# Optimization experiments

Hardware: AMD Instinct MI355X
Metric: run time of the kernel (lower is better)

Reference implementation:

```python
import jax, jax.numpy as jnp
import numpy as np

B, D, H, W = 4, 64, 64, 64
MODES = 8
WIDTH = 32
N_LAYERS = 4


def setup_inputs() -> dict:
    key = jax.random.key(0)
    ks = jax.random.split(key, 20)
    C = WIDTH
    m = MODES
    spec_scale = 1.0 / (C * C)
    inp = {
        "velocity_model": jax.random.normal(ks[0], (B, 1, D, H, W), jnp.float32),
        "partial_travel_time": jax.random.normal(ks[1], (B, 1, D, H, W), jnp.float32),
        "lift_w": jax.random.normal(ks[2], (2, C), jnp.float32) * 0.5,
        "lift_b": jax.random.normal(ks[3], (C,), jnp.float32) * 0.1,
        "spec_wr": jax.random.normal(ks[4], (N_LAYERS, 4, C, C, m, m, m), jnp.float32) * spec_scale,
        "spec_wi": jax.random.normal(ks[5], (N_LAYERS, 4, C, C, m, m, m), jnp.float32) * spec_scale,
        "skip_w": jax.random.normal(ks[6], (N_LAYERS, C, C), jnp.float32) * (1.0 / np.sqrt(C)),
        "skip_b": jax.random.normal(ks[7], (N_LAYERS, C), jnp.float32) * 0.1,
        "proj_w": jax.random.normal(ks[8], (C, C), jnp.float32) * (1.0 / np.sqrt(C)),
        "proj_b": jax.random.normal(ks[9], (C,), jnp.float32) * 0.1,
        "fc1_w": jax.random.normal(ks[10], (C, 128), jnp.float32) * (1.0 / np.sqrt(C)),
        "fc1_b": jax.random.normal(ks[11], (128,), jnp.float32) * 0.1,
        "fc2_w": jax.random.normal(ks[12], (128, 64), jnp.float32) * (1.0 / np.sqrt(128)),
        "fc2_b": jax.random.normal(ks[13], (64,), jnp.float32) * 0.1,
        "fc3_w": jax.random.normal(ks[14], (64, 3), jnp.float32) * (1.0 / np.sqrt(64)),
        "fc3_b": jax.random.normal(ks[15], (3,), jnp.float32) * 0.1,
    }
    return inp


def _spectral_conv3d(x, wr, wi, m):
    # x: [B, Cin, D, H, W] real; wr/wi: [4, Cin, Cout, m, m, m]
    b, ci, d, h, w = x.shape
    co = wr.shape[2]
    xf = jnp.fft.rfftn(x, axes=(-3, -2, -1))  # [B, Cin, D, H, W//2+1] complex
    wc = wr + 1j * wi
    lo = slice(None, m)
    hi = slice(-m, None)
    corners = [(lo, lo), (lo, hi), (hi, lo), (hi, hi)]
    out = jnp.zeros((b, co, d, h, w // 2 + 1), dtype=xf.dtype)
    for i, (sd, sh) in enumerate(corners):
        blk = jnp.einsum('bixyz,ioxyz->boxyz', xf[:, :, sd, sh, :m], wc[i])
        out = out.at[:, :, sd, sh, :m].set(blk)
    return jnp.fft.irfftn(out, s=(d, h, w), axes=(-3, -2, -1))


def _channel_linear(x, w, bias):
    # x: [B, Cin, D, H, W]; w: [Cin, Cout]
    return jnp.einsum('bixyz,io->boxyz', x, w) + bias[None, :, None, None, None]


def reference(velocity_model, partial_travel_time, lift_w, lift_b, spec_wr, spec_wi,
              skip_w, skip_b, proj_w, proj_b, fc1_w, fc1_b, fc2_w, fc2_b, fc3_w, fc3_b):
    # concat along channel dim -> [B, 2, D, H, W]
    x = jnp.concatenate([velocity_model, partial_travel_time], axis=1)
    # lifting to hidden width
    x = _channel_linear(x, lift_w, lift_b)
    n_layers = spec_wr.shape[0]
    for l in range(n_layers):
        y = _spectral_conv3d(x, spec_wr[l], spec_wi[l], MODES)
        s = _channel_linear(x, skip_w[l], skip_b[l])
        x = y + s
        if l < n_layers - 1:
            x = jax.nn.gelu(x)
    # projection to out_channels = width
    x = _channel_linear(x, proj_w, proj_b)
    # global spatial mean -> [B, width]
    x = jnp.mean(x, axis=(-3, -2, -1))
    # MLP head: width -> 128 -> 64 -> 3
    x = jax.nn.relu(x @ fc1_w + fc1_b)
    x = jax.nn.relu(x @ fc2_w + fc2_b)
    return x @ fc3_w + fc3_b
```

## Files before the change

### kernel.cpp

```cpp
#include <hip/hip_runtime.h>
#include <math.h>

#define NSP 262144
static constexpr float TWO_PI_OVER_64 = 0.09817477042468103f;

__global__ __launch_bounds__(256) void k_fwd_wh2(const float* __restrict__ vel,
                                                 const float* __restrict__ ptt,
                                                 float2* __restrict__ VP2) {
  __shared__ float plane[64][65];
  __shared__ float2 A[64][8];
  __shared__ float2 tw[64];
  int t = threadIdx.x;
  if (t < 64) { float s, c; sincosf(TWO_PI_OVER_64 * t, &s, &c); tw[t] = make_float2(c, s); }
  int b = blockIdx.x >> 7, ch = (blockIdx.x >> 6) & 1, d = blockIdx.x & 63;
  const float4* src = (const float4*)((ch ? ptt : vel) + (size_t)b * NSP + d * 4096);
  for (int p = 0; p < 4; ++p) {
    int i = t + 256 * p;
    float4 v = src[i];
    int h = i >> 4, sg = (i & 15) * 4;
    plane[h][sg] = v.x; plane[h][sg + 1] = v.y; plane[h][sg + 2] = v.z; plane[h][sg + 3] = v.w;
  }
  __syncthreads();
  for (int p = 0; p < 2; ++p) {
    int o = t + 256 * p;
    int h = o >> 3, kw = o & 7;
    float re = 0.f, im = 0.f;
    for (int w = 0; w < 64; ++w) {
      float2 cs = tw[(kw * w) & 63];
      float v = plane[h][w];
      re += v * cs.x; im -= v * cs.y;
    }
    A[h][kw] = make_float2(re, im);
  }
  __syncthreads();
  if (t < 128) {
    int kh = t >> 3, kw = t & 7;
    int f = (kh < 8) ? kh : kh + 48;
    float re = 0.f, im = 0.f;
    for (int h = 0; h < 64; ++h) {
      float2 cs = tw[(h * f) & 63];
      float2 a = A[h][kw];
      re += a.x * cs.x + a.y * cs.y;
      im += a.y * cs.x - a.x * cs.y;
    }
    VP2[(size_t)blockIdx.x * 128 + t] = make_float2(re, im);
  }
}

__global__ __launch_bounds__(256) void k_fwd_d_lift(const float2* __restrict__ VP2,
                                                    const float* __restrict__ lw,
                                                    const float* __restrict__ lb,
                                                    float2* __restrict__ X3) {
  __shared__ float2 tile[2][64][8];
  __shared__ float2 F[2][16][8];
  __shared__ float2 tw[64];
  int t = threadIdx.x;
  if (t < 64) { float s, c; sincosf(TWO_PI_OVER_64 * t, &s, &c); tw[t] = make_float2(c, s); }
  int b = blockIdx.x >> 4, kh = blockIdx.x & 15;
  for (int p = 0; p < 4; ++p) {
    int i = t + 256 * p;
    int ch = i >> 9, dd = (i >> 3) & 63, kw = i & 7;
    tile[ch][dd][kw] = VP2[(size_t)((b * 2 + ch) * 64 + dd) * 128 + kh * 8 + kw];
  }
  __syncthreads();
  { int ch = t >> 7, kd = (t >> 3) & 15, kw = t & 7;
    int f = (kd < 8) ? kd : kd + 48;
    float re = 0.f, im = 0.f;
    for (int dd = 0; dd < 64; ++dd) {
      float2 cs = tw[(dd * f) & 63];
      float2 v = tile[ch][dd][kw];
      re += v.x * cs.x + v.y * cs.y;
      im += v.y * cs.x - v.x * cs.y;
    }
    F[ch][kd][kw] = make_float2(re, im); }
  __syncthreads();
  for (int p = 0; p < 16; ++p) {
    int o = t + 256 * p;
    int ci = o >> 7, kd = (o >> 3) & 15, kw = o & 7;
    float2 f0 = F[0][kd][kw], f1 = F[1][kd][kw];
    float w0 = lw[ci], w1 = lw[32 + ci];
    float2 v = make_float2(w0 * f0.x + w1 * f1.x, w0 * f0.y + w1 * f1.y);
    if (kh == 0 && kd == 0 && kw == 0) v.x += lb[ci] * 262144.f;
    X3[(size_t)(b * 32 + ci) * 2048 + kd * 128 + kh * 8 + kw] = v;
  }
}

__global__ __launch_bounds__(128) void k_fwd_h(const float2* __restrict__ X1,
                                               float2* __restrict__ X2) {
  __shared__ float2 tile[64][8];
  __shared__ float2 tw[64];
  int t = threadIdx.x;
  if (t < 64) { float s, c; sincosf(TWO_PI_OVER_64 * t, &s, &c); tw[t] = make_float2(c, s); }
  const float4* s4 = (const float4*)(X1 + (size_t)blockIdx.x * 512);
  float4* t4 = (float4*)tile;
  t4[t] = s4[t];
  t4[t + 128] = s4[t + 128];
  __syncthreads();
  int kh = t >> 3, k = t & 7;
  int f = (kh < 8) ? kh : kh + 48;
  float re = 0.f, im = 0.f;
#pragma unroll 8
  for (int h = 0; h < 64; ++h) {
    float2 cs = tw[(h * f) & 63];
    float2 v = tile[h][k];
    re += v.x * cs.x + v.y * cs.y;
    im += v.y * cs.x - v.x * cs.y;
  }
  X2[(size_t)blockIdx.x * 128 + t] = make_float2(re, im);
}

__global__ __launch_bounds__(128) void k_fwd_d(const float2* __restrict__ X2,
                                               float2* __restrict__ X3) {
  __shared__ float2 tile[64][8];
  __shared__ float2 tw[64];
  int t = threadIdx.x;
  if (t < 64) { float s, c; sincosf(TWO_PI_OVER_64 * t, &s, &c); tw[t] = make_float2(c, s); }
  int kh = blockIdx.x & 15, bc = blockIdx.x >> 4;
  const float2* src = X2 + (size_t)bc * 8192 + kh * 8;
  for (int i = t; i < 512; i += 128) tile[i >> 3][i & 7] = src[(i >> 3) * 128 + (i & 7)];
  __syncthreads();
  int kd = t >> 3, k = t & 7;
  int f = (kd < 8) ? kd : kd + 48;
  float re = 0.f, im = 0.f;
#pragma unroll 8
  for (int d = 0; d < 64; ++d) {
    float2 cs = tw[(d * f) & 63];
    float2 v = tile[d][k];
    re += v.x * cs.x + v.y * cs.y;
    im += v.y * cs.x - v.x * cs.y;
  }
  X3[(size_t)bc * 2048 + kd * 128 + kh * 8 + k] = make_float2(re, im);
}

__global__ __launch_bounds__(256) void k_mix(const float2* __restrict__ X3,
                                             const float* __restrict__ wr,
                                             const float* __restrict__ wi,
                                             float2* __restrict__ Y3) {
  __shared__ float2 xs[4][32][8];
  int t = threadIdx.x;
  int kd = blockIdx.x >> 4, kh = blockIdx.x & 15;
  for (int i = t; i < 1024; i += 256) {
    int b = i >> 8, ci = (i >> 3) & 31, k = i & 7;
    xs[b][ci][k] = X3[(size_t)(b * 32 + ci) * 2048 + kd * 128 + kh * 8 + k];
  }
  __syncthreads();
  int corner = ((kd >= 8) ? 2 : 0) + ((kh >= 8) ? 1 : 0);
  int md = kd & 7, mh = kh & 7;
  int co = t >> 3, k = t & 7;
  size_t wbase = (size_t)corner * 32 * 32 * 512 + (size_t)md * 64 + (size_t)mh * 8 + k;
  float ar0 = 0, ai0 = 0, ar1 = 0, ai1 = 0, ar2 = 0, ai2 = 0, ar3 = 0, ai3 = 0;
  for (int ci = 0; ci < 32; ++ci) {
    size_t o = wbase + (size_t)(ci * 32 + co) * 512;
    float wre = wr[o], wim = wi[o];
    float2 v0 = xs[0][ci][k], v1 = xs[1][ci][k];
    float2 v2 = xs[2][ci][k], v3 = xs[3][ci][k];
    ar0 += v0.x * wre - v0.y * wim;  ai0 += v0.x * wim + v0.y * wre;
    ar1 += v1.x * wre - v1.y * wim;  ai1 += v1.x * wim + v1.y * wre;
    ar2 += v2.x * wre - v2.y * wim;  ai2 += v2.x * wim + v2.y * wre;
    ar3 += v3.x * wre - v3.y * wim;  ai3 += v3.x * wim + v3.y * wre;
  }
  size_t obase = (size_t)kd * 128 + kh * 8 + k;
  Y3[(size_t)(0 * 32 + co) * 2048 + obase] = make_float2(ar0, ai0);
  Y3[(size_t)(1 * 32 + co) * 2048 + obase] = make_float2(ar1, ai1);
  Y3[(size_t)(2 * 32 + co) * 2048 + obase] = make_float2(ar2, ai2);
  Y3[(size_t)(3 * 32 + co) * 2048 + obase] = make_float2(ar3, ai3);
}

__global__ __launch_bounds__(256) void k_inv_dh(const float2* __restrict__ Y3,
                                                float2* __restrict__ Z2) {
  __shared__ float2 yt[2048];
  __shared__ float2 zd[4][16][8];
  __shared__ float2 tw[64];
  int t = threadIdx.x;
  if (t < 64) { float s, c; sincosf(TWO_PI_OVER_64 * t, &s, &c); tw[t] = make_float2(c, s); }
  int bc = blockIdx.x >> 4, d0 = (blockIdx.x & 15) * 4;
  const float4* y4 = (const float4*)(Y3 + (size_t)bc * 2048);
  float4* yt4 = (float4*)yt;
  for (int p = 0; p < 4; ++p) yt4[t + 256 * p] = y4[t + 256 * p];
  __syncthreads();
  const float sc = 1.f / 262144.f;
  for (int p = 0; p < 2; ++p) {
    int o = t + 256 * p;
    int dd = o >> 7, kh = (o >> 3) & 15, kw = o & 7;
    int d = d0 + dd;
    float re = 0.f, im = 0.f;
#pragma unroll
    for (int kd = 0; kd < 16; ++kd) {
      int f = (kd < 8) ? kd : kd + 48;
      float2 cs = tw[(d * f) & 63];
      float2 v = yt[kd * 128 + kh * 8 + kw];
      re += v.x * cs.x - v.y * cs.y;
      im += v.x * cs.y + v.y * cs.x;
    }
    zd[dd][kh][kw] = make_float2(re * sc, im * sc);
  }
  __syncthreads();
  for (int p = 0; p < 8; ++p) {
    int o = t + 256 * p;
    int dd = o >> 9, h = (o >> 3) & 63, kw = o & 7;
    float re = 0.f, im = 0.f;
#pragma unroll
    for (int kh = 0; kh < 16; ++kh) {
      int f = (kh < 8) ? kh : kh + 48;
      float2 cs = tw[(h * f) & 63];
      float2 v = zd[dd][kh][kw];
      re += v.x * cs.x - v.y * cs.y;
      im += v.x * cs.y + v.y * cs.x;
    }
    Z2[((size_t)bc * 64 + d0 + dd) * 512 + h * 8 + kw] = make_float2(re, im);
  }
}

template <int MODE>
__global__ __launch_bounds__(256, 3) void k_tail(
    const float2* __restrict__ S, const float* __restrict__ xin,
    const float* __restrict__ pttin, const float* __restrict__ lw,
    const float* __restrict__ lb, const float* __restrict__ skw,
    const float* __restrict__ skb, float* __restrict__ xout,
    float2* __restrict__ X1out, float* __restrict__ pr) {
  __shared__ float2 tw[64];
  __shared__ float2 zt[32][2][9];
  __shared__ float sw[32][32];
  __shared__ float xt[(MODE == 0) ? 2 : 32][2][64];
  __shared__ float gt[(MODE == 2) ? 1 : 32][2][68];
  int t = threadIdx.x;
  if (t < 64) { float s, c; sincosf(TWO_PI_OVER_64 * t, &s, &c); tw[t] = make_float2(c, s); }
  int b = blockIdx.x >> 11, d = (blockIdx.x >> 5) & 63, h0 = (blockIdx.x & 31) * 2;
  {
    int co = t >> 3, hh = (t >> 2) & 1, q = t & 3;
    const float4* S4 = (const float4*)S;
    float4 v = S4[(size_t)((b * 32 + co) * 64 + d) * 256 + (h0 + hh) * 4 + q];
    zt[co][hh][2 * q] = make_float2(v.x, v.y);
    zt[co][hh][2 * q + 1] = make_float2(v.z, v.w);
  }
  if constexpr (MODE == 0) {
    if (t < 64) {
      int ch = t >> 5, hh = (t >> 4) & 1, sg = t & 15;
      const float4* src = (const float4*)(ch ? pttin : xin);
      *(float4*)&xt[ch][hh][sg * 4] =
          src[((size_t)b * NSP + d * 4096 + (h0 + hh) * 64) / 4 + sg];
    } else if (t >= 128 && t < 192) {
      int j = (t >> 5) & 1, co = t & 31;
      float a = 0.f;
      for (int ci = 0; ci < 32; ++ci) a += lw[j * 32 + ci] * skw[ci * 32 + co];
      sw[j][co] = a;
    } else if (t >= 192 && t < 224) {
      int co = t & 31;
      float a = skb[co];
      for (int ci = 0; ci < 32; ++ci) a += lb[ci] * skw[ci * 32 + co];
      sw[2][co] = a;
    }
  } else {
    { int ci = t >> 3, q = t & 7;
      *(float4*)&sw[ci][q * 4] = ((const float4*)skw)[t]; }
    for (int p = 0; p < 4; ++p) {
      int idx = t + 256 * p, row = idx >> 4, ci = row >> 1, hh = row & 1, sg = idx & 15;
      *(float4*)&xt[ci][hh][sg * 4] =
          ((const float4*)xin)[(size_t)(((b * 32 + ci) * 64 + d) * 64 + h0 + hh) * 16 + sg];
    }
  }
  __syncthreads();

  int co = t >> 3, ws = t & 7;
  float bias = (MODE == 0) ? sw[2][co] : skb[co];
  float acc[2][8];
#pragma unroll
  for (int hh = 0; hh < 2; ++hh) {
    float z0 = zt[co][hh][0].x;
#pragma unroll
    for (int j = 0; j < 8; ++j) acc[hh][j] = bias + z0;
  }
#pragma unroll
  for (int k = 1; k < 8; ++k) {
    float2 z0 = zt[co][0][k], z1 = zt[co][1][k];
#pragma unroll
    for (int j = 0; j < 8; ++j) {
      float2 cs = tw[(k * (8 * ws + j)) & 63];
      acc[0][j] += 2.f * (z0.x * cs.x - z0.y * cs.y);
      acc[1][j] += 2.f * (z1.x * cs.x - z1.y * cs.y);
    }
  }
  constexpr int NCI = (MODE == 0) ? 2 : 32;
  for (int ci = 0; ci < NCI; ++ci) {
    float s = sw[ci][co];
#pragma unroll
    for (int hh = 0; hh < 2; ++hh) {
      float4 a = *(const float4*)&xt[ci][hh][8 * ws];
      float4 c2 = *(const float4*)&xt[ci][hh][8 * ws + 4];
      acc[hh][0] += a.x * s;  acc[hh][1] += a.y * s;
      acc[hh][2] += a.z * s;  acc[hh][3] += a.w * s;
      acc[hh][4] += c2.x * s; acc[hh][5] += c2.y * s;
      acc[hh][6] += c2.z * s; acc[hh][7] += c2.w * s;
    }
  }
#pragma unroll
  for (int hh = 0; hh < 2; ++hh)
#pragma unroll
    for (int j = 0; j < 8; ++j) {
      float g = acc[hh][j];
      float u = 0.7978845608028654f * (g + 0.044715f * g * g * g);
      acc[hh][j] = __fdividef(g, 1.f + __expf(-2.f * u));
    }

  if constexpr (MODE == 2) {
    float s = 0.f;
#pragma unroll
    for (int hh = 0; hh < 2; ++hh)
#pragma unroll
      for (int j = 0; j < 8; ++j) s += acc[hh][j];
    s += __shfl_down(s, 4, 8);
    s += __shfl_down(s, 2, 8);
    s += __shfl_down(s, 1, 8);
    if (ws == 0) atomicAdd(&pr[b * 32 + co], s);
  } else {
#pragma unroll
    for (int hh = 0; hh < 2; ++hh) {
      *(float4*)&gt[co][hh][8 * ws] = make_float4(acc[hh][0], acc[hh][1], acc[hh][2], acc[hh][3]);
      *(float4*)&gt[co][hh][8 * ws + 4] = make_float4(acc[hh][4], acc[hh][5], acc[hh][6], acc[hh][7]);
    }
    __syncthreads();
    for (int p = 0; p < 4; ++p) {
      int idx = t + 256 * p, row = idx >> 4, ci = row >> 1, hh = row & 1, sg = idx & 15;
      ((float4*)xout)[(size_t)(((b * 32 + ci) * 64 + d) * 64 + h0 + hh) * 16 + sg] =
          *(float4*)&gt[ci][hh][sg * 4];
    }
    for (int p = 0; p < 2; ++p) {
      int o = t + 256 * p;
      int c2 = o >> 4, hh = (o >> 3) & 1, kw = o & 7;
      float re = 0.f, im = 0.f;
      for (int w = 0; w < 64; ++w) {
        float g = gt[c2][hh][w];
        float2 cs = tw[(kw * w) & 63];
        re += g * cs.x;
        im -= g * cs.y;
      }
      X1out[(size_t)((b * 32 + c2) * 64 + d) * 512 + (h0 + hh) * 8 + kw] = make_float2(re, im);
    }
  }
}

__global__ __launch_bounds__(128) void k_head(const float* __restrict__ pr,
                                              const float* __restrict__ swr,
                                              const float* __restrict__ skw,
                                              const float* __restrict__ skb,
                                              const float* __restrict__ pw,
                                              const float* __restrict__ pb,
                                              const float* __restrict__ f1w,
                                              const float* __restrict__ f1b,
                                              const float* __restrict__ f2w,
                                              const float* __restrict__ f2b,
                                              const float* __restrict__ f3w,
                                              const float* __restrict__ f3b,
                                              float* __restrict__ out) {
  __shared__ float m[128], h1[128], p2[128], f1[512], f2[256];
  int t = threadIdx.x;
  m[t] = pr[t] * (1.f / 262144.f);
  __syncthreads();
  { int b = t >> 5, co = t & 31;
    float acc = skb[96 + co];
    for (int ci = 0; ci < 32; ++ci) {
      float wdc = swr[((size_t)12 * 1024 + (size_t)(ci * 32 + co)) * 512];
      acc += m[b * 32 + ci] * (wdc + skw[3072 + ci * 32 + co]);
    }
    h1[t] = acc; }
  __syncthreads();
  { int b = t >> 5, o = t & 31;
    float acc = pb[o];
    for (int c = 0; c < 32; ++c) acc += h1[b * 32 + c] * pw[c * 32 + o];
    p2[t] = acc; }
  __syncthreads();
  for (int j = 0; j < 4; ++j) {
    int idx = t + 128 * j, b = idx >> 7, o = idx & 127;
    float acc = f1b[o];
    for (int c = 0; c < 32; ++c) acc += p2[b * 32 + c] * f1w[c * 128 + o];
    f1[idx] = fmaxf(acc, 0.f);
  }
  __syncthreads();
  for (int j = 0; j < 2; ++j) {
    int idx = t + 128 * j, b = idx >> 6, o = idx & 63;
    float acc = f2b[o];
    for (int c = 0; c < 128; ++c) acc += f1[b * 128 + c] * f2w[c * 64 + o];
    f2[idx] = fmaxf(acc, 0.f);
  }
  __syncthreads();
  if (t < 12) {
    int b = t / 3, o = t % 3;
    float acc = f3b[o];
    for (int c = 0; c < 64; ++c) acc += f2[b * 64 + c] * f3w[c * 3 + o];
    out[t] = acc;
  }
}

extern "C" void kernel_launch(void* const* d_in, const int* in_sizes, int n_in,
                              void* d_out, int out_size, void* d_ws, size_t ws_size,
                              hipStream_t stream) {
  const float* vel = (const float*)d_in[0];
  const float* ptt = (const float*)d_in[1];
  const float* lw  = (const float*)d_in[2];
  const float* lb  = (const float*)d_in[3];
  const float* swr = (const float*)d_in[4];
  const float* swi = (const float*)d_in[5];
  const float* skw = (const float*)d_in[6];
  const float* skb = (const float*)d_in[7];
  const float* pw  = (const float*)d_in[8];
  const float* pb  = (const float*)d_in[9];
  const float* f1w = (const float*)d_in[10];
  const float* f1b = (const float*)d_in[11];
  const float* f2w = (const float*)d_in[12];
  const float* f2b = (const float*)d_in[13];
  const float* f3w = (const float*)d_in[14];
  const float* f3b = (const float*)d_in[15];
  float* out = (float*)d_out;

  char* ws = (char*)d_ws;
  float*  x   = (float*)(ws);
  float2* S   = (float2*)(ws + 134217728ULL);
  float2* X2  = (float2*)(ws + 167772160ULL);
  float2* VP2 = X2;
  float2* X3  = (float2*)(ws + 176160768ULL);
  float2* Y3  = (float2*)(ws + 178257920ULL);
  float*  pr  = (float*)(ws + 180355072ULL);
  if (ws_size < 180355584ULL) return;

  hipMemsetAsync(pr, 0, 512, stream);

  k_fwd_wh2<<<512, 256, 0, stream>>>(vel, ptt, VP2);
  k_fwd_d_lift<<<64, 256, 0, stream>>>(VP2, lw, lb, X3);
  k_mix<<<256, 256, 0, stream>>>(X3, swr, swi, Y3);
  k_inv_dh<<<2048, 256, 0, stream>>>(Y3, S);
  k_tail<0><<<8192, 256, 0, stream>>>(S, vel, ptt, lw, lb, skw, skb, x, S, nullptr);

  k_fwd_h<<<8192, 128, 0, stream>>>(S, X2);
  k_fwd_d<<<2048, 128, 0, stream>>>(X2, X3);
  k_mix<<<256, 256, 0, stream>>>(X3, swr + 2097152, swi + 2097152, Y3);
  k_inv_dh<<<2048, 256, 0, stream>>>(Y3, S);
  k_tail<1><<<8192, 256, 0, stream>>>(S, x, nullptr, nullptr, nullptr,
                                      skw + 1024, skb + 32, x, S, nullptr);

  k_fwd_h<<<8192, 128, 0, stream>>>(S, X2);
  k_fwd_d<<<2048, 128, 0, stream>>>(X2, X3);
  k_mix<<<256, 256, 0, stream>>>(X3, swr + 2 * 2097152, swi + 2 * 2097152, Y3);
  k_inv_dh<<<2048, 256, 0, stream>>>(Y3, S);
  k_tail<2><<<8192, 256, 0, stream>>>(S, x, nullptr, nullptr, nullptr,
                                      skw + 2048, skb + 64, nullptr, nullptr, pr);

  k_head<<<1, 128, 0, stream>>>(pr, swr, skw, skb, pw, pb, f1w, f1b,
                                f2w, f2b, f3w, f3b, out);
}
```

Measured before the change: 724.2 us.

## Register-tile k_tail over 8 channels by 8 w, with shuffle-based partial DFT

Restructures the tail kernel so each thread computes an 8-channel by 8-width register tile, covering 4 h rows per block with 128 threads. Twiddles come from recurrence multiplication instead of table lookups. The forward W-DFT of the output is done in registers and reduced with warp butterfly shuffles rather than through a shared gt buffer and a 64-long loop per output. This aims to cut shared-memory traffic and per-element twiddle loads, at the cost of much higher register pressure (launch bounds 128,1) and lower occupancy.

```diff
diff --git a/kernel.cpp b/kernel.cpp
--- a/kernel.cpp
+++ b/kernel.cpp
@@ -212,129 +212,216 @@
 }
 
 template <int MODE>
-__global__ __launch_bounds__(256, 3) void k_tail(
+__global__ __launch_bounds__(128, 1) void k_tail(
     const float2* __restrict__ S, const float* __restrict__ xin,
     const float* __restrict__ pttin, const float* __restrict__ lw,
     const float* __restrict__ lb, const float* __restrict__ skw,
     const float* __restrict__ skb, float* __restrict__ xout,
-    float2* __restrict__ X1out, float* __restrict__ pr) {
-  __shared__ float2 tw[64];
-  __shared__ float2 zt[32][2][9];
-  __shared__ float sw[32][32];
-  __shared__ float xt[(MODE == 0) ? 2 : 32][2][64];
-  __shared__ float gt[(MODE == 2) ? 1 : 32][2][68];
-  int t = threadIdx.x;
-  if (t < 64) { float s, c; sincosf(TWO_PI_OVER_64 * t, &s, &c); tw[t] = make_float2(c, s); }
-  int b = blockIdx.x >> 11, d = (blockIdx.x >> 5) & 63, h0 = (blockIdx.x & 31) * 2;
+    float2* __restrict__ Sout, float* __restrict__ pr) {
+  __shared__ float2 zt[4][8][32];
+  __shared__ float xt[(MODE == 0) ? 2 : 32][4][64];
+  __shared__ float sw[(MODE == 0) ? 3 : 32][32];
+  __shared__ float2 tws[64];
+  int t = threadIdx.x;
+  if (t < 64) { float s, c; sincosf(TWO_PI_OVER_64 * t, &s, &c); tws[t] = make_float2(c, s); }
+  int b = blockIdx.x >> 10, d = (blockIdx.x >> 4) & 63, ht = blockIdx.x & 15;
+
   {
-    int co = t >> 3, hh = (t >> 2) & 1, q = t & 3;
+    int co = t >> 2, sub = t & 3;
     const float4* S4 = (const float4*)S;
-    float4 v = S4[(size_t)((b * 32 + co) * 64 + d) * 256 + (h0 + hh) * 4 + q];
-    zt[co][hh][2 * q] = make_float2(v.x, v.y);
-    zt[co][hh][2 * q + 1] = make_float2(v.z, v.w);
+    size_t base = ((size_t)(b * 32 + co) * 64 + d) * 256;
+#pragma unroll
+    for (int hl = 0; hl < 4; ++hl) {
+      float4 v = S4[base + (ht * 4 + hl) * 4 + sub];
+      zt[hl][2 * sub][co] = make_float2(v.x, v.y);
+      zt[hl][2 * sub + 1][co] = make_float2(v.z, v.w);
+    }
   }
   if constexpr (MODE == 0) {
-    if (t < 64) {
-      int ch = t >> 5, hh = (t >> 4) & 1, sg = t & 15;
+    { int ch = t >> 6, hl = (t >> 4) & 3, q = t & 15;
       const float4* src = (const float4*)(ch ? pttin : xin);
-      *(float4*)&xt[ch][hh][sg * 4] =
-          src[((size_t)b * NSP + d * 4096 + (h0 + hh) * 64) / 4 + sg];
-    } else if (t >= 128 && t < 192) {
-      int j = (t >> 5) & 1, co = t & 31;
-      float a = 0.f;
-      for (int ci = 0; ci < 32; ++ci) a += lw[j * 32 + ci] * skw[ci * 32 + co];
-      sw[j][co] = a;
-    } else if (t >= 192 && t < 224) {
-      int co = t & 31;
-      float a = skb[co];
-      for (int ci = 0; ci < 32; ++ci) a += lb[ci] * skw[ci * 32 + co];
-      sw[2][co] = a;
+      *(float4*)&xt[ch][hl][q * 4] =
+          src[(size_t)b * 65536 + d * 1024 + (ht * 4 + hl) * 16 + q]; }
+    if (t < 96) {
+      int r = t >> 5, co = t & 31;
+      if (r < 2) {
+        float a = 0.f;
+        for (int ci = 0; ci < 32; ++ci) a += lw[r * 32 + ci] * skw[ci * 32 + co];
+        sw[r][co] = a;
+      } else {
+        float a = skb[co];
+        for (int ci = 0; ci < 32; ++ci) a += lb[ci] * skw[ci * 32 + co];
+        sw[2][co] = a;
+      }
     }
   } else {
-    { int ci = t >> 3, q = t & 7;
-      *(float4*)&sw[ci][q * 4] = ((const float4*)skw)[t]; }
-    for (int p = 0; p < 4; ++p) {
-      int idx = t + 256 * p, row = idx >> 4, ci = row >> 1, hh = row & 1, sg = idx & 15;
-      *(float4*)&xt[ci][hh][sg * 4] =
-          ((const float4*)xin)[(size_t)(((b * 32 + ci) * 64 + d) * 64 + h0 + hh) * 16 + sg];
-    }
-  }
-  __syncthreads();
-
-  int co = t >> 3, ws = t & 7;
-  float bias = (MODE == 0) ? sw[2][co] : skb[co];
-  float acc[2][8];
-#pragma unroll
-  for (int hh = 0; hh < 2; ++hh) {
-    float z0 = zt[co][hh][0].x;
-#pragma unroll
-    for (int j = 0; j < 8; ++j) acc[hh][j] = bias + z0;
+    ((float4*)sw)[t] = ((const float4*)skw)[t];
+    ((float4*)sw)[t + 128] = ((const float4*)skw)[t + 128];
+    { int ci = t >> 2, q = t & 3;
+      const float4* x4 = (const float4*)xin;
+      size_t base = (((size_t)(b * 32 + ci) * 64 + d) * 64 + ht * 4) * 16;
+#pragma unroll
+      for (int hl = 0; hl < 4; ++hl)
+#pragma unroll
+        for (int j = 0; j < 4; ++j)
+          *(float4*)&xt[ci][hl][(q + 4 * j) * 4] = x4[base + hl * 16 + q + 4 * j];
+    }
+  }
+  __syncthreads();
+
+  int cg = t >> 5, hloc = (t >> 3) & 3, ws = t & 7;
+  int co0 = cg * 8, h = ht * 4 + hloc, w0 = ws * 8;
+  float2 e1[8], cur[8];
+#pragma unroll
+  for (int j = 0; j < 8; ++j) { e1[j] = tws[w0 + j]; cur[j] = e1[j]; }
+  float bias[8];
+#pragma unroll
+  for (int r = 0; r < 8; ++r)
+    bias[r] = (MODE == 0) ? sw[2][co0 + r] : skb[co0 + r];
+
+  float g[8][8];
+  {
+    const float4* zp = (const float4*)&zt[hloc][0][co0];
+    float4 a0 = zp[0], a1 = zp[1], a2 = zp[2], a3 = zp[3];
+    float z0[8] = {a0.x, a0.z, a1.x, a1.z, a2.x, a2.z, a3.x, a3.z};
+#pragma unroll
+    for (int r = 0; r < 8; ++r) {
+      float v = z0[r] + bias[r];
+#pragma unroll
+      for (int j = 0; j < 8; ++j) g[r][j] = v;
+    }
   }
 #pragma unroll
   for (int k = 1; k < 8; ++k) {
-    float2 z0 = zt[co][0][k], z1 = zt[co][1][k];
+    const float4* zp = (const float4*)&zt[hloc][k][co0];
+    float4 a0 = zp[0], a1 = zp[1], a2 = zp[2], a3 = zp[3];
+    float2 z[8] = {make_float2(a0.x, a0.y), make_float2(a0.z, a0.w),
+                   make_float2(a1.x, a1.y), make_float2(a1.z, a1.w),
+                   make_float2(a2.x, a2.y), make_float2(a2.z, a2.w),
+                   make_float2(a3.x, a3.y), make_float2(a3.z, a3.w)};
+#pragma unroll
+    for (int r = 0; r < 8; ++r)
+#pragma unroll
+      for (int j = 0; j < 8; ++j)
+        g[r][j] += 2.f * (z[r].x * cur[j].x - z[r].y * cur[j].y);
+    if (k < 7)
+#pragma unroll
+      for (int j = 0; j < 8; ++j) {
+        float cx = cur[j].x * e1[j].x - cur[j].y * e1[j].y;
+        cur[j].y = cur[j].x * e1[j].y + cur[j].y * e1[j].x;
+        cur[j].x = cx;
+      }
+  }
+  constexpr int NCI = (MODE == 0) ? 2 : 32;
+#pragma unroll
+  for (int ci = 0; ci < NCI; ++ci) {
+    float4 xa = *(const float4*)&xt[ci][hloc][w0];
+    float4 xb = *(const float4*)&xt[ci][hloc][w0 + 4];
+    float4 sa = *(const float4*)&sw[ci][co0];
+    float4 sb = *(const float4*)&sw[ci][co0 + 4];
+    float xv[8] = {xa.x, xa.y, xa.z, xa.w, xb.x, xb.y, xb.z, xb.w};
+    float sv[8] = {sa.x, sa.y, sa.z, sa.w, sb.x, sb.y, sb.z, sb.w};
+#pragma unroll
+    for (int r = 0; r < 8; ++r)
+#pragma unroll
+      for (int j = 0; j < 8; ++j) g[r][j] += xv[j] * sv[r];
+  }
+#pragma unroll
+  for (int r = 0; r < 8; ++r)
 #pragma unroll
     for (int j = 0; j < 8; ++j) {
-      float2 cs = tw[(k * (8 * ws + j)) & 63];
-      acc[0][j] += 2.f * (z0.x * cs.x - z0.y * cs.y);
-      acc[1][j] += 2.f * (z1.x * cs.x - z1.y * cs.y);
-    }
-  }
-  constexpr int NCI = (MODE == 0) ? 2 : 32;
-  for (int ci = 0; ci < NCI; ++ci) {
-    float s = sw[ci][co];
-#pragma unroll
-    for (int hh = 0; hh < 2; ++hh) {
-      float4 a = *(const float4*)&xt[ci][hh][8 * ws];
-      float4 c2 = *(const float4*)&xt[ci][hh][8 * ws + 4];
-      acc[hh][0] += a.x * s;  acc[hh][1] += a.y * s;
-      acc[hh][2] += a.z * s;  acc[hh][3] += a.w * s;
-      acc[hh][4] += c2.x * s; acc[hh][5] += c2.y * s;
-      acc[hh][6] += c2.z * s; acc[hh][7] += c2.w * s;
-    }
-  }
-#pragma unroll
-  for (int hh = 0; hh < 2; ++hh)
-#pragma unroll
-    for (int j = 0; j < 8; ++j) {
-      float g = acc[hh][j];
-      float u = 0.7978845608028654f * (g + 0.044715f * g * g * g);
-      acc[hh][j] = __fdividef(g, 1.f + __expf(-2.f * u));
+      float v = g[r][j];
+      float u = 0.7978845608028654f * (v + 0.044715f * v * v * v);
+      g[r][j] = __fdividef(v, 1.f + __expf(-2.f * u));
     }
 
   if constexpr (MODE == 2) {
-    float s = 0.f;
-#pragma unroll
-    for (int hh = 0; hh < 2; ++hh)
-#pragma unroll
-      for (int j = 0; j < 8; ++j) s += acc[hh][j];
-    s += __shfl_down(s, 4, 8);
-    s += __shfl_down(s, 2, 8);
-    s += __shfl_down(s, 1, 8);
-    if (ws == 0) atomicAdd(&pr[b * 32 + co], s);
+    float rs[8];
+#pragma unroll
+    for (int r = 0; r < 8; ++r) {
+      float s = 0.f;
+#pragma unroll
+      for (int j = 0; j < 8; ++j) s += g[r][j];
+      rs[r] = s;
+    }
+#pragma unroll
+    for (int off = 1; off < 32; off <<= 1)
+#pragma unroll
+      for (int r = 0; r < 8; ++r) rs[r] += __shfl_xor(rs[r], off, 32);
+    if ((t & 31) == 0)
+#pragma unroll
+      for (int r = 0; r < 8; ++r) atomicAdd(&pr[b * 32 + co0 + r], rs[r]);
   } else {
-#pragma unroll
-    for (int hh = 0; hh < 2; ++hh) {
-      *(float4*)&gt[co][hh][8 * ws] = make_float4(acc[hh][0], acc[hh][1], acc[hh][2], acc[hh][3]);
-      *(float4*)&gt[co][hh][8 * ws + 4] = make_float4(acc[hh][4], acc[hh][5], acc[hh][6], acc[hh][7]);
-    }
-    __syncthreads();
-    for (int p = 0; p < 4; ++p) {
-      int idx = t + 256 * p, row = idx >> 4, ci = row >> 1, hh = row & 1, sg = idx & 15;
-      ((float4*)xout)[(size_t)(((b * 32 + ci) * 64 + d) * 64 + h0 + hh) * 16 + sg] =
-          *(float4*)&gt[ci][hh][sg * 4];
-    }
-    for (int p = 0; p < 2; ++p) {
-      int o = t + 256 * p;
-      int c2 = o >> 4, hh = (o >> 3) & 1, kw = o & 7;
-      float re = 0.f, im = 0.f;
-      for (int w = 0; w < 64; ++w) {
-        float g = gt[c2][hh][w];
-        float2 cs = tw[(kw * w) & 63];
-        re += g * cs.x;
-        im -= g * cs.y;
+    float4* x4o = (float4*)xout;
+#pragma unroll
+    for (int r = 0; r < 8; ++r) {
+      size_t o = (((size_t)(b * 32 + co0 + r) * 64 + d) * 64 + h) * 16 + 2 * ws;
+      x4o[o] = make_float4(g[r][0], g[r][1], g[r][2], g[r][3]);
+      x4o[o + 1] = make_float4(g[r][4], g[r][5], g[r][6], g[r][7]);
+    }
+#pragma unroll
+    for (int half = 0; half < 2; ++half) {
+      float2 P[4][8];
+#pragma unroll
+      for (int r = 0; r < 4; ++r) {
+        float s = 0.f;
+#pragma unroll
+        for (int j = 0; j < 8; ++j) s += g[half * 4 + r][j];
+        P[r][0] = make_float2(s, 0.f);
       }
-      X1out[(size_t)((b * 32 + c2) * 64 + d) * 512 + (h0 + hh) * 8 + kw] = make_float2(re, im);
+      float2 cc[8];
+#pragma unroll
+      for (int j = 0; j < 8; ++j) cc[j] = make_float2(e1[j].x, -e1[j].y);
+#pragma unroll
+      for (int kw = 1; kw < 8; ++kw) {
+#pragma unroll
+        for (int r = 0; r < 4; ++r) {
+          float re = 0.f, im = 0.f;
+#pragma unroll
+          for (int j = 0; j < 8; ++j) {
+            re += g[half * 4 + r][j] * cc[j].x;
+            im += g[half * 4 + r][j] * cc[j].y;
+          }
+          P[r][kw] = make_float2(re, im);
+        }
+        if (kw < 7)
+#pragma unroll
+          for (int j = 0; j < 8; ++j) {
+            float cx = cc[j].x * e1[j].x + cc[j].y * e1[j].y;
+            cc[j].y = cc[j].y * e1[j].x - cc[j].x * e1[j].y;
+            cc[j].x = cx;
+          }
+      }
+      float2 Q[4][4];
+#pragma unroll
+      for (int r = 0; r < 4; ++r)
+#pragma unroll
+        for (int kk = 0; kk < 4; ++kk) {
+          float2 keep = (ws & 4) ? P[r][kk + 4] : P[r][kk];
+          float2 send = (ws & 4) ? P[r][kk] : P[r][kk + 4];
+          keep.x += __shfl_xor(send.x, 4, 8);
+          keep.y += __shfl_xor(send.y, 4, 8);
+          Q[r][kk] = keep;
+        }
+      float2 R[4][2];
+#pragma unroll
+      for (int r = 0; r < 4; ++r)
+#pragma unroll
+        for (int kk = 0; kk < 2; ++kk) {
+          float2 keep = (ws & 2) ? Q[r][kk + 2] : Q[r][kk];
+          float2 send = (ws & 2) ? Q[r][kk] : Q[r][kk + 2];
+          keep.x += __shfl_xor(send.x, 2, 8);
+          keep.y += __shfl_xor(send.y, 2, 8);
+          R[r][kk] = keep;
+        }
+#pragma unroll
+      for (int r = 0; r < 4; ++r) {
+        float2 keep = (ws & 1) ? R[r][1] : R[r][0];
+        float2 send = (ws & 1) ? R[r][0] : R[r][1];
+        keep.x += __shfl_xor(send.x, 1, 8);
+        keep.y += __shfl_xor(send.y, 1, 8);
+        Sout[((size_t)(b * 32 + co0 + half * 4 + r) * 64 + d) * 512 + h * 8 + ws] = keep;
+      }
     }
   }
 }
@@ -428,20 +515,20 @@
   k_fwd_d_lift<<<64, 256, 0, stream>>>(VP2, lw, lb, X3);
   k_mix<<<256, 256, 0, stream>>>(X3, swr, swi, Y3);
   k_inv_dh<<<2048, 256, 0, stream>>>(Y3, S);
-  k_tail<0><<<8192, 256, 0, stream>>>(S, vel, ptt, lw, lb, skw, skb, x, S, nullptr);
+  k_tail<0><<<4096, 128, 0, stream>>>(S, vel, ptt, lw, lb, skw, skb, x, S, nullptr);
 
   k_fwd_h<<<8192, 128, 0, stream>>>(S, X2);
   k_fwd_d<<<2048, 128, 0, stream>>>(X2, X3);
   k_mix<<<256, 256, 0, stream>>>(X3, swr + 2097152, swi + 2097152, Y3);
   k_inv_dh<<<2048, 256, 0, stream>>>(Y3, S);
-  k_tail<1><<<8192, 256, 0, stream>>>(S, x, nullptr, nullptr, nullptr,
+  k_tail<1><<<4096, 128, 0, stream>>>(S, x, nullptr, nullptr, nullptr,
                                       skw + 1024, skb + 32, x, S, nullptr);
 
   k_fwd_h<<<8192, 128, 0, stream>>>(S, X2);
   k_fwd_d<<<2048, 128, 0, stream>>>(X2, X3);
   k_mix<<<256, 256, 0, stream>>>(X3, swr + 2 * 2097152, swi + 2 * 2097152, Y3);
   k_inv_dh<<<2048, 256, 0, stream>>>(Y3, S);
-  k_tail<2><<<8192, 256, 0, stream>>>(S, x, nullptr, nullptr, nullptr,
+  k_tail<2><<<4096, 128, 0, stream>>>(S, x, nullptr, nullptr, nullptr,
                                       skw + 2048, skb + 64, nullptr, nullptr, pr);
 
   k_head<<<1, 128, 0, stream>>>(pr, swr, skw, skb, pw, pb, f1w, f1b,
```

After: 930.3 us. 28.5% more time.

## Use twiddle recurrences and shuffle-based W-DFT in tail kernel, drop smem staging

Applied to the files above, without the earlier changes.

The H and D forward DFT kernels now generate twiddles by complex multiplication recurrence instead of indexed shared-memory lookups. In k_tail, the inverse-W twiddles are produced by recurrence from per-thread base factors. The forward W-DFT of the GELU output is computed in registers as per-thread partial sums, then reduced across the 8 lanes with a butterfly of xor shuffles. This removes the gt shared staging buffer and one __syncthreads, and xout is written directly from registers. Occupancy is raised to 4 blocks per SM. The recurrences add floating-point rounding drift, and the change raises register pressure.

```diff
diff --git a/kernel.cpp b/kernel.cpp
--- a/kernel.cpp
+++ b/kernel.cpp
@@ -98,13 +98,17 @@
   __syncthreads();
   int kh = t >> 3, k = t & 7;
   int f = (kh < 8) ? kh : kh + 48;
+  float2 E = tw[f];
+  float2 cur = make_float2(1.f, 0.f);
   float re = 0.f, im = 0.f;
 #pragma unroll 8
   for (int h = 0; h < 64; ++h) {
-    float2 cs = tw[(h * f) & 63];
     float2 v = tile[h][k];
-    re += v.x * cs.x + v.y * cs.y;
-    im += v.y * cs.x - v.x * cs.y;
+    re += v.x * cur.x + v.y * cur.y;
+    im += v.y * cur.x - v.x * cur.y;
+    float cx = cur.x * E.x - cur.y * E.y;
+    cur.y = cur.x * E.y + cur.y * E.x;
+    cur.x = cx;
   }
   X2[(size_t)blockIdx.x * 128 + t] = make_float2(re, im);
 }
@@ -121,13 +125,17 @@
   __syncthreads();
   int kd = t >> 3, k = t & 7;
   int f = (kd < 8) ? kd : kd + 48;
+  float2 E = tw[f];
+  float2 cur = make_float2(1.f, 0.f);
   float re = 0.f, im = 0.f;
 #pragma unroll 8
   for (int d = 0; d < 64; ++d) {
-    float2 cs = tw[(d * f) & 63];
     float2 v = tile[d][k];
-    re += v.x * cs.x + v.y * cs.y;
-    im += v.y * cs.x - v.x * cs.y;
+    re += v.x * cur.x + v.y * cur.y;
+    im += v.y * cur.x - v.x * cur.y;
+    float cx = cur.x * E.x - cur.y * E.y;
+    cur.y = cur.x * E.y + cur.y * E.x;
+    cur.x = cx;
   }
   X3[(size_t)bc * 2048 + kd * 128 + kh * 8 + k] = make_float2(re, im);
 }
@@ -212,19 +220,18 @@
 }
 
 template <int MODE>
-__global__ __launch_bounds__(256, 3) void k_tail(
+__global__ __launch_bounds__(256, 4) void k_tail(
     const float2* __restrict__ S, const float* __restrict__ xin,
     const float* __restrict__ pttin, const float* __restrict__ lw,
     const float* __restrict__ lb, const float* __restrict__ skw,
     const float* __restrict__ skb, float* __restrict__ xout,
-    float2* __restrict__ X1out, float* __restrict__ pr) {
-  __shared__ float2 tw[64];
+    float2* __restrict__ Sout, float* __restrict__ pr) {
+  __shared__ float2 tws[64];
   __shared__ float2 zt[32][2][9];
-  __shared__ float sw[32][32];
+  __shared__ float sw[(MODE == 0) ? 3 : 32][32];
   __shared__ float xt[(MODE == 0) ? 2 : 32][2][64];
-  __shared__ float gt[(MODE == 2) ? 1 : 32][2][68];
-  int t = threadIdx.x;
-  if (t < 64) { float s, c; sincosf(TWO_PI_OVER_64 * t, &s, &c); tw[t] = make_float2(c, s); }
+  int t = threadIdx.x;
+  if (t < 64) { float s, c; sincosf(TWO_PI_OVER_64 * t, &s, &c); tws[t] = make_float2(c, s); }
   int b = blockIdx.x >> 11, d = (blockIdx.x >> 5) & 63, h0 = (blockIdx.x & 31) * 2;
   {
     int co = t >> 3, hh = (t >> 2) & 1, q = t & 3;
@@ -262,44 +269,59 @@
   __syncthreads();
 
   int co = t >> 3, ws = t & 7;
+  float2 e1[8];
+#pragma unroll
+  for (int j = 0; j < 8; ++j) e1[j] = tws[8 * ws + j];
   float bias = (MODE == 0) ? sw[2][co] : skb[co];
+
   float acc[2][8];
-#pragma unroll
-  for (int hh = 0; hh < 2; ++hh) {
-    float z0 = zt[co][hh][0].x;
-#pragma unroll
-    for (int j = 0; j < 8; ++j) acc[hh][j] = bias + z0;
-  }
-#pragma unroll
-  for (int k = 1; k < 8; ++k) {
-    float2 z0 = zt[co][0][k], z1 = zt[co][1][k];
-#pragma unroll
-    for (int j = 0; j < 8; ++j) {
-      float2 cs = tw[(k * (8 * ws + j)) & 63];
-      acc[0][j] += 2.f * (z0.x * cs.x - z0.y * cs.y);
-      acc[1][j] += 2.f * (z1.x * cs.x - z1.y * cs.y);
+  {
+    float z00 = zt[co][0][0].x, z10 = zt[co][1][0].x;
+#pragma unroll
+    for (int j = 0; j < 8; ++j) { acc[0][j] = bias + z00; acc[1][j] = bias + z10; }
+  }
+  {
+    float2 cur[8];
+#pragma unroll
+    for (int j = 0; j < 8; ++j) cur[j] = e1[j];
+#pragma unroll
+    for (int k = 1; k < 8; ++k) {
+      float2 z0 = zt[co][0][k], z1 = zt[co][1][k];
+#pragma unroll
+      for (int j = 0; j < 8; ++j) {
+        acc[0][j] += 2.f * (z0.x * cur[j].x - z0.y * cur[j].y);
+        acc[1][j] += 2.f * (z1.x * cur[j].x - z1.y * cur[j].y);
+      }
+      if (k < 7)
+#pragma unroll
+        for (int j = 0; j < 8; ++j) {
+          float cx = cur[j].x * e1[j].x - cur[j].y * e1[j].y;
+          cur[j].y = cur[j].x * e1[j].y + cur[j].y * e1[j].x;
+          cur[j].x = cx;
+        }
     }
   }
   constexpr int NCI = (MODE == 0) ? 2 : 32;
+#pragma unroll 4
   for (int ci = 0; ci < NCI; ++ci) {
     float s = sw[ci][co];
 #pragma unroll
     for (int hh = 0; hh < 2; ++hh) {
-      float4 a = *(const float4*)&xt[ci][hh][8 * ws];
-      float4 c2 = *(const float4*)&xt[ci][hh][8 * ws + 4];
-      acc[hh][0] += a.x * s;  acc[hh][1] += a.y * s;
-      acc[hh][2] += a.z * s;  acc[hh][3] += a.w * s;
-      acc[hh][4] += c2.x * s; acc[hh][5] += c2.y * s;
-      acc[hh][6] += c2.z * s; acc[hh][7] += c2.w * s;
+      float4 xa = *(const float4*)&xt[ci][hh][8 * ws];
+      float4 xb = *(const float4*)&xt[ci][hh][8 * ws + 4];
+      acc[hh][0] += xa.x * s;  acc[hh][1] += xa.y * s;
+      acc[hh][2] += xa.z * s;  acc[hh][3] += xa.w * s;
+      acc[hh][4] += xb.x * s;  acc[hh][5] += xb.y * s;
+      acc[hh][6] += xb.z * s;  acc[hh][7] += xb.w * s;
     }
   }
 #pragma unroll
   for (int hh = 0; hh < 2; ++hh)
 #pragma unroll
     for (int j = 0; j < 8; ++j) {
-      float g = acc[hh][j];
-      float u = 0.7978845608028654f * (g + 0.044715f * g * g * g);
-      acc[hh][j] = __fdividef(g, 1.f + __expf(-2.f * u));
+      float v = acc[hh][j];
+      float u = 0.7978845608028654f * (v + 0.044715f * v * v * v);
+      acc[hh][j] = __fdividef(v, 1.f + __expf(-2.f * u));
     }
 
   if constexpr (MODE == 2) {
@@ -313,28 +335,63 @@
     s += __shfl_down(s, 1, 8);
     if (ws == 0) atomicAdd(&pr[b * 32 + co], s);
   } else {
+    float4* x4o = (float4*)xout;
 #pragma unroll
     for (int hh = 0; hh < 2; ++hh) {
-      *(float4*)&gt[co][hh][8 * ws] = make_float4(acc[hh][0], acc[hh][1], acc[hh][2], acc[hh][3]);
-      *(float4*)&gt[co][hh][8 * ws + 4] = make_float4(acc[hh][4], acc[hh][5], acc[hh][6], acc[hh][7]);
-    }
-    __syncthreads();
-    for (int p = 0; p < 4; ++p) {
-      int idx = t + 256 * p, row = idx >> 4, ci = row >> 1, hh = row & 1, sg = idx & 15;
-      ((float4*)xout)[(size_t)(((b * 32 + ci) * 64 + d) * 64 + h0 + hh) * 16 + sg] =
-          *(float4*)&gt[ci][hh][sg * 4];
-    }
-    for (int p = 0; p < 2; ++p) {
-      int o = t + 256 * p;
-      int c2 = o >> 4, hh = (o >> 3) & 1, kw = o & 7;
-      float re = 0.f, im = 0.f;
-      for (int w = 0; w < 64; ++w) {
-        float g = gt[c2][hh][w];
-        float2 cs = tw[(kw * w) & 63];
-        re += g * cs.x;
-        im -= g * cs.y;
+      size_t o = (((size_t)(b * 32 + co) * 64 + d) * 64 + h0 + hh) * 16 + 2 * ws;
+      x4o[o]     = make_float4(acc[hh][0], acc[hh][1], acc[hh][2], acc[hh][3]);
+      x4o[o + 1] = make_float4(acc[hh][4], acc[hh][5], acc[hh][6], acc[hh][7]);
+    }
+    float2 P[2][8];
+#pragma unroll
+    for (int hh = 0; hh < 2; ++hh)
+#pragma unroll
+      for (int kw = 0; kw < 8; ++kw) P[hh][kw] = make_float2(0.f, 0.f);
+#pragma unroll
+    for (int j = 0; j < 8; ++j) {
+      float2 cc = make_float2(e1[j].x, -e1[j].y);
+      float2 cur = make_float2(1.f, 0.f);
+      float g0 = acc[0][j], g1 = acc[1][j];
+#pragma unroll
+      for (int kw = 0; kw < 8; ++kw) {
+        P[0][kw].x += g0 * cur.x;  P[0][kw].y += g0 * cur.y;
+        P[1][kw].x += g1 * cur.x;  P[1][kw].y += g1 * cur.y;
+        if (kw < 7) {
+          float cx = cur.x * cc.x - cur.y * cc.y;
+          cur.y = cur.x * cc.y + cur.y * cc.x;
+          cur.x = cx;
+        }
       }
-      X1out[(size_t)((b * 32 + c2) * 64 + d) * 512 + (h0 + hh) * 8 + kw] = make_float2(re, im);
+    }
+    float2 Q[2][4];
+#pragma unroll
+    for (int hh = 0; hh < 2; ++hh)
+#pragma unroll
+      for (int kk = 0; kk < 4; ++kk) {
+        float2 keep = (ws & 4) ? P[hh][kk + 4] : P[hh][kk];
+        float2 send = (ws & 4) ? P[hh][kk] : P[hh][kk + 4];
+        keep.x += __shfl_xor(send.x, 4);
+        keep.y += __shfl_xor(send.y, 4);
+        Q[hh][kk] = keep;
+      }
+    float2 R[2][2];
+#pragma unroll
+    for (int hh = 0; hh < 2; ++hh)
+#pragma unroll
+      for (int kk = 0; kk < 2; ++kk) {
+        float2 keep = (ws & 2) ? Q[hh][kk + 2] : Q[hh][kk];
+        float2 send = (ws & 2) ? Q[hh][kk] : Q[hh][kk + 2];
+        keep.x += __shfl_xor(send.x, 2);
+        keep.y += __shfl_xor(send.y, 2);
+        R[hh][kk] = keep;
+      }
+#pragma unroll
+    for (int hh = 0; hh < 2; ++hh) {
+      float2 keep = (ws & 1) ? R[hh][1] : R[hh][0];
+      float2 send = (ws & 1) ? R[hh][0] : R[hh][1];
+      keep.x += __shfl_xor(send.x, 1);
+      keep.y += __shfl_xor(send.y, 1);
+      Sout[((size_t)(b * 32 + co) * 64 + d) * 512 + (h0 + hh) * 8 + ws] = keep;
     }
   }
 }
```

Result: no change. 738.1 us (+1.9%).
